# Optimization experiments

Hardware: AMD Instinct MI355X
Metric: run time of the kernel (lower is better)

Reference implementation:

```python
import jax, jax.numpy as jnp
import numpy as np

N = 50000      # nodes
E = 800000     # edges (avg degree 16)
DIN = 128
DOUT = 128
L = 8          # num GCN2Conv layers
ALPHA = 0.1
THETA = 0.5


def setup_inputs() -> dict:
    key = jax.random.key(0)
    ks = jax.random.split(key, 5)
    x = jax.random.normal(ks[0], (N, DIN), jnp.float32)
    edge_index = jax.random.randint(ks[1], (2, E), 0, N, dtype=jnp.int64)
    # pre-normalized adjacency weights (normalize=False in GCN2Conv -> adj_t already normalized)
    edge_weight = jax.random.uniform(ks[2], (E,), jnp.float32) / 16.0
    W_lin = jax.random.normal(ks[3], (DIN, DOUT), jnp.float32) / np.sqrt(DIN).astype(np.float32)
    b_lin = jnp.zeros((DOUT,), jnp.float32)
    W_convs = jax.random.normal(ks[4], (L, DOUT, DOUT), jnp.float32) / np.sqrt(DOUT).astype(np.float32)
    return {"x": x, "edge_weight": edge_weight, "W_lin": W_lin, "b_lin": b_lin,
            "W_convs": W_convs, "edge_index": edge_index}


def reference(x, edge_weight, W_lin, b_lin, W_convs, edge_index):
    src, dst = edge_index[0], edge_index[1]
    # betas for GCN2Conv layer l (1-indexed): beta_l = log(theta/l + 1)
    betas = np.log(THETA / np.arange(1, L + 1) + 1.0).astype(np.float32)
    # x = lins(x).relu(); dropout p=0 is a no-op
    x0 = jax.nn.relu(x @ W_lin + b_lin)          # [N, DOUT]
    h = x0
    for l in range(L):
        # sparse propagate: agg = A @ h  (SpMM via gather + segment_sum)
        agg = jax.ops.segment_sum(h[src] * edge_weight[:, None], dst, num_segments=N)
        # initial-residual mixing
        m = (1.0 - ALPHA) * agg + ALPHA * x0
        # identity mapping (shared_weights): out = (1-beta)*m + beta*(m @ W)
        h = jax.nn.relu((1.0 - betas[l]) * m + betas[l] * (m @ W_convs[l]))
    return h
```

## Files before the change

### kernel.cpp

```cpp
#include <hip/hip_runtime.h>
#include <math.h>

#define N_NODES 50000
#define N_EDGES 800000
#define DIM 128
#define SCAN_BLOCKS 49

typedef __attribute__((ext_vector_type(8))) short short8;
typedef __attribute__((ext_vector_type(4))) float floatx4;

__device__ __forceinline__ unsigned short f32_to_bf16(float f) {
    unsigned int u = __float_as_uint(f);
    u += 0x7fffu + ((u >> 16) & 1u);
    return (unsigned short)(u >> 16);
}
__device__ __forceinline__ float bf16_to_f32(unsigned short h) {
    return __uint_as_float((unsigned int)h << 16);
}


__global__ __launch_bounds__(256) void hist_kernel(const int* __restrict__ dst,
                                                   int* __restrict__ deg) {
    int e = blockIdx.x * 256 + threadIdx.x;
    if (e < N_EDGES) atomicAdd(&deg[dst[e]], 1);
}

__global__ __launch_bounds__(1024) void scan1(const int* __restrict__ deg,
                                              int* __restrict__ rowp,
                                              int* __restrict__ part) {
    __shared__ int buf[1024];
    int i = blockIdx.x * 1024 + threadIdx.x;
    int v = (i < N_NODES) ? deg[i] : 0;
    buf[threadIdx.x] = v;
    __syncthreads();
    for (int off = 1; off < 1024; off <<= 1) {
        int t = (threadIdx.x >= (unsigned)off) ? buf[threadIdx.x - off] : 0;
        __syncthreads();
        buf[threadIdx.x] += t;
        __syncthreads();
    }
    if (i < N_NODES) rowp[i] = buf[threadIdx.x] - v;
    if (threadIdx.x == 1023) part[blockIdx.x] = buf[1023];
}

__global__ void scan2(int* __restrict__ part) {
    int v = (threadIdx.x < SCAN_BLOCKS) ? part[threadIdx.x] : 0;
    for (int off = 1; off < 64; off <<= 1) {
        int t = __shfl_up(v, off);
        if ((int)threadIdx.x >= off) v += t;
    }
    if (threadIdx.x < SCAN_BLOCKS) part[threadIdx.x] = v;
}

__global__ __launch_bounds__(1024) void scan3(int* __restrict__ rowp,
                                              int* __restrict__ cursor,
                                              const int* __restrict__ part) {
    int i = blockIdx.x * 1024 + threadIdx.x;
    int off = (blockIdx.x > 0) ? part[blockIdx.x - 1] : 0;
    if (i < N_NODES) {
        int r = rowp[i] + off;
        rowp[i] = r;
        cursor[i] = r;
    }
    if (i == N_NODES) rowp[N_NODES] = part[SCAN_BLOCKS - 1];
}

__global__ __launch_bounds__(256) void scatter_kernel(const int* __restrict__ src,
                                                      const int* __restrict__ dst,
                                                      const float* __restrict__ ew,
                                                      int* __restrict__ cursor,
                                                      int2* __restrict__ ep) {
    int e = blockIdx.x * 256 + threadIdx.x;
    if (e < N_EDGES) {
        int d = dst[e];
        int pos = atomicAdd(&cursor[d], 1);
        int2 p; p.x = src[e]; p.y = __float_as_int(ew[e]);
        ep[pos] = p;
    }
}


__global__ __launch_bounds__(256) void spmm7(const unsigned short* __restrict__ hB,
                                             const unsigned short* __restrict__ x0B,
                                             const int* __restrict__ rowp,
                                             const int2* __restrict__ ep,
                                             unsigned short* __restrict__ mB) {
    int node = blockIdx.x * 4 + (threadIdx.x >> 6);
    int lane = threadIdx.x & 63;
    int eg = lane >> 4;
    int fb = (lane & 15) * 8;
    int beg = rowp[node], end = rowp[node + 1];
    float acc[8] = {0.f, 0.f, 0.f, 0.f, 0.f, 0.f, 0.f, 0.f};
    if (beg < end) {
        int last = end - 1;
        for (int i = beg; i < end; i += 16) {
            int i0 = i + eg, i1 = i0 + 4, i2 = i0 + 8, i3 = i0 + 12;
            int2 e0 = ep[min(i0, last)];
            int2 e1 = ep[min(i1, last)];
            int2 e2 = ep[min(i2, last)];
            int2 e3 = ep[min(i3, last)];
            short8 r0 = *(const short8*)(const void*)(hB + (size_t)e0.x * DIM + fb);
            short8 r1 = *(const short8*)(const void*)(hB + (size_t)e1.x * DIM + fb);
            short8 r2 = *(const short8*)(const void*)(hB + (size_t)e2.x * DIM + fb);
            short8 r3 = *(const short8*)(const void*)(hB + (size_t)e3.x * DIM + fb);
            float w0 = (i0 < end) ? __int_as_float(e0.y) : 0.f;
            float w1 = (i1 < end) ? __int_as_float(e1.y) : 0.f;
            float w2 = (i2 < end) ? __int_as_float(e2.y) : 0.f;
            float w3 = (i3 < end) ? __int_as_float(e3.y) : 0.f;
#pragma unroll
            for (int j = 0; j < 8; j++) {
                acc[j] = fmaf(w0, bf16_to_f32((unsigned short)r0[j]), acc[j]);
                acc[j] = fmaf(w1, bf16_to_f32((unsigned short)r1[j]), acc[j]);
                acc[j] = fmaf(w2, bf16_to_f32((unsigned short)r2[j]), acc[j]);
                acc[j] = fmaf(w3, bf16_to_f32((unsigned short)r3[j]), acc[j]);
            }
        }
    }
#pragma unroll
    for (int j = 0; j < 8; j++) {
        acc[j] += __shfl_down(acc[j], 32);
        acc[j] += __shfl_down(acc[j], 16);
    }
    if (lane < 16) {
        size_t off = (size_t)node * DIM + fb;
        short8 xv = *(const short8*)(const void*)(x0B + off);
        short8 o;
#pragma unroll
        for (int j = 0; j < 8; j++)
            o[j] = (short)f32_to_bf16(0.9f * acc[j]
                                      + 0.1f * bf16_to_f32((unsigned short)xv[j]));
        *(short8*)(void*)(mB + off) = o;
    }
}


template <bool AF32>
__global__ __launch_bounds__(256) void gemm128(const void* __restrict__ Av,
                                               const float* __restrict__ W,
                                               const float* __restrict__ bias,
                                               float* __restrict__ outF,
                                               unsigned short* __restrict__ outB,
                                               float cm, float cg) {
    __shared__ unsigned short WT[128][136];
    for (int idx = threadIdx.x; idx < 128 * 128; idx += 256) {
        int k = idx >> 7, n = idx & 127;
        float wv = cg * W[idx] + ((n == k) ? cm : 0.f);
        WT[n][k] = f32_to_bf16(wv);
    }
    __syncthreads();

    int wave = threadIdx.x >> 6;
    int lane = threadIdx.x & 63;
    int r0 = (blockIdx.x * 4 + wave) * 16;
    if (r0 >= N_NODES) return;

    int mrow = lane & 15;
    int quad = lane >> 4;

    floatx4 acc[8];
#pragma unroll
    for (int t = 0; t < 8; t++) acc[t] = {0.f, 0.f, 0.f, 0.f};

#pragma unroll
    for (int k0 = 0; k0 < 128; k0 += 32) {
        short8 a;
        if constexpr (AF32) {
            const float* arow = (const float*)Av + (size_t)(r0 + mrow) * DIM;
            floatx4 alo = *(const floatx4*)(const void*)(arow + k0 + quad * 8);
            floatx4 ahi = *(const floatx4*)(const void*)(arow + k0 + quad * 8 + 4);
#pragma unroll
            for (int j = 0; j < 4; j++) a[j] = (short)f32_to_bf16(alo[j]);
#pragma unroll
            for (int j = 0; j < 4; j++) a[4 + j] = (short)f32_to_bf16(ahi[j]);
        } else {
            const unsigned short* arow = (const unsigned short*)Av + (size_t)(r0 + mrow) * DIM;
            a = *(const short8*)(const void*)(arow + k0 + quad * 8);
        }
#pragma unroll
        for (int t = 0; t < 8; t++) {
            short8 b = *(const short8*)(const void*)(&WT[t * 16 + mrow][k0 + quad * 8]);
            acc[t] = __builtin_amdgcn_mfma_f32_16x16x32_bf16(a, b, acc[t], 0, 0, 0);
        }
    }

#pragma unroll
    for (int t = 0; t < 8; t++) {
        int col = t * 16 + mrow;
        float bv = bias ? bias[col] : 0.f;
#pragma unroll
        for (int i = 0; i < 4; i++) {
            int row = r0 + quad * 4 + i;
            size_t off = (size_t)row * DIM + col;
            float v = fmaxf(acc[t][i] + bv, 0.f);
            if (outF) outF[off] = v;
            if (outB) outB[off] = f32_to_bf16(v);
        }
    }
}


extern "C" void kernel_launch(void* const* d_in, const int* in_sizes, int n_in,
                              void* d_out, int out_size, void* d_ws, size_t ws_size,
                              hipStream_t stream) {
    const float* x    = (const float*)d_in[0];
    const float* ew   = (const float*)d_in[1];
    const float* Wlin = (const float*)d_in[2];
    const float* blin = (const float*)d_in[3];
    const float* Wcv  = (const float*)d_in[4];
    const int* eidx = (const int*)d_in[5];
    const int* esrc = eidx;
    const int* edst = eidx + N_EDGES;
    float* out = (float*)d_out;

    char* ws = (char*)d_ws;
    unsigned short* x0B = (unsigned short*)(ws);
    unsigned short* mB  = (unsigned short*)(ws + 12800000);
    unsigned short* hB  = (unsigned short*)(ws + 25600000);
    int* rowp           = (int*)(ws + 38400000);
    int* cursor         = (int*)(ws + 38600064);
    int2* epack         = (int2*)(ws + 38800128);
    int* part           = (int*)(ws + 45200128);

    (void)hipMemsetAsync(cursor, 0, (N_NODES + 1) * sizeof(int), stream);
    hist_kernel<<<(N_EDGES + 255) / 256, 256, 0, stream>>>(edst, cursor);
    scan1<<<SCAN_BLOCKS, 1024, 0, stream>>>(cursor, rowp, part);
    scan2<<<1, 64, 0, stream>>>(part);
    scan3<<<SCAN_BLOCKS, 1024, 0, stream>>>(rowp, cursor, part);
    scatter_kernel<<<(N_EDGES + 255) / 256, 256, 0, stream>>>(esrc, edst, ew, cursor, epack);

    const int grid = (N_NODES + 63) / 64;

    gemm128<true><<<grid, 256, 0, stream>>>(x, Wlin, blin, nullptr, x0B, 0.f, 1.f);

    const unsigned short* hin = x0B;
    for (int l = 0; l < 8; l++) {
        spmm7<<<N_NODES / 4, 256, 0, stream>>>(hin, x0B, rowp, epack, mB);
        float beta = logf(0.5f / (float)(l + 1) + 1.f);
        gemm128<false><<<grid, 256, 0, stream>>>(mB, Wcv + (size_t)l * DIM * DIM, nullptr,
                                                 (l == 7) ? out : nullptr,
                                                 (l < 7) ? hB : nullptr,
                                                 1.f - beta, beta);
        hin = hB;
    }
}
```

Before: 550.3 us.

## Fuse SpMM aggregation with per-layer GEMM and precompute bf16 layer weights

```diff
diff --git a/kernel.cpp b/kernel.cpp
--- a/kernel.cpp
+++ b/kernel.cpp
@@ -75,77 +75,126 @@
         int d = dst[e];
         int pos = atomicAdd(&cursor[d], 1);
         int2 p; p.x = src[e]; p.y = __float_as_int(ew[e]);
-        ep[pos] = p;
-    }
-}
-
-
-__global__ __launch_bounds__(256) void spmm7(const unsigned short* __restrict__ hB,
-                                             const unsigned short* __restrict__ x0B,
-                                             const int* __restrict__ rowp,
-                                             const int2* __restrict__ ep,
-                                             unsigned short* __restrict__ mB) {
-    int node = blockIdx.x * 4 + (threadIdx.x >> 6);
+        long long pv;
+        __builtin_memcpy(&pv, &p, 8);
+        __builtin_nontemporal_store(pv, (long long*)(ep + pos));
+    }
+}
+
+
+__global__ __launch_bounds__(256) void prep_wt(const float* __restrict__ Wcv,
+                                               unsigned short* __restrict__ WTall) {
+    int l = blockIdx.x;
+    float beta = logf(0.5f / (float)(l + 1) + 1.f);
+    float cm = 1.f - beta, cg = beta;
+    const float* W = Wcv + (size_t)l * DIM * DIM;
+    unsigned short* WT = WTall + (size_t)l * DIM * DIM;
+    for (int idx = threadIdx.x; idx < DIM * DIM; idx += 256) {
+        int k = idx >> 7, n = idx & 127;
+        WT[n * DIM + k] = f32_to_bf16(cg * W[idx] + ((n == k) ? cm : 0.f));
+    }
+}
+
+
+__global__ __launch_bounds__(256) void layer_fused(const unsigned short* __restrict__ hB,
+                                                   const unsigned short* __restrict__ x0B,
+                                                   const int* __restrict__ rowp,
+                                                   const int2* __restrict__ ep,
+                                                   const unsigned short* __restrict__ WT,
+                                                   float* __restrict__ outF,
+                                                   unsigned short* __restrict__ outB) {
+    __shared__ unsigned short M[16][136];
+    int wave = threadIdx.x >> 6;
     int lane = threadIdx.x & 63;
     int eg = lane >> 4;
     int fb = (lane & 15) * 8;
-    int beg = rowp[node], end = rowp[node + 1];
-    float acc[8] = {0.f, 0.f, 0.f, 0.f, 0.f, 0.f, 0.f, 0.f};
-    if (beg < end) {
-        int last = end - 1;
-        for (int i = beg; i < end; i += 16) {
-            int i0 = i + eg, i1 = i0 + 4, i2 = i0 + 8, i3 = i0 + 12;
-            int2 e0 = ep[min(i0, last)];
-            int2 e1 = ep[min(i1, last)];
-            int2 e2 = ep[min(i2, last)];
-            int2 e3 = ep[min(i3, last)];
-            short8 r0 = *(const short8*)(const void*)(hB + (size_t)e0.x * DIM + fb);
-            short8 r1 = *(const short8*)(const void*)(hB + (size_t)e1.x * DIM + fb);
-            short8 r2 = *(const short8*)(const void*)(hB + (size_t)e2.x * DIM + fb);
-            short8 r3 = *(const short8*)(const void*)(hB + (size_t)e3.x * DIM + fb);
-            float w0 = (i0 < end) ? __int_as_float(e0.y) : 0.f;
-            float w1 = (i1 < end) ? __int_as_float(e1.y) : 0.f;
-            float w2 = (i2 < end) ? __int_as_float(e2.y) : 0.f;
-            float w3 = (i3 < end) ? __int_as_float(e3.y) : 0.f;
-#pragma unroll
-            for (int j = 0; j < 8; j++) {
-                acc[j] = fmaf(w0, bf16_to_f32((unsigned short)r0[j]), acc[j]);
-                acc[j] = fmaf(w1, bf16_to_f32((unsigned short)r1[j]), acc[j]);
-                acc[j] = fmaf(w2, bf16_to_f32((unsigned short)r2[j]), acc[j]);
-                acc[j] = fmaf(w3, bf16_to_f32((unsigned short)r3[j]), acc[j]);
+    int nodeBase = blockIdx.x * 16;
+
+    for (int t = 0; t < 4; t++) {
+        int nl = wave * 4 + t;
+        int node = nodeBase + nl;
+        int beg = rowp[node], end = rowp[node + 1];
+        float acc[8] = {0.f, 0.f, 0.f, 0.f, 0.f, 0.f, 0.f, 0.f};
+        if (beg < end) {
+            int last = end - 1;
+            for (int i = beg; i < end; i += 16) {
+                int i0 = i + eg, i1 = i0 + 4, i2 = i0 + 8, i3 = i0 + 12;
+                int2 e0 = ep[min(i0, last)];
+                int2 e1 = ep[min(i1, last)];
+                int2 e2 = ep[min(i2, last)];
+                int2 e3 = ep[min(i3, last)];
+                short8 r0 = *(const short8*)(const void*)(hB + (size_t)e0.x * DIM + fb);
+                short8 r1 = *(const short8*)(const void*)(hB + (size_t)e1.x * DIM + fb);
+                short8 r2 = *(const short8*)(const void*)(hB + (size_t)e2.x * DIM + fb);
+                short8 r3 = *(const short8*)(const void*)(hB + (size_t)e3.x * DIM + fb);
+                float w0 = (i0 < end) ? __int_as_float(e0.y) : 0.f;
+                float w1 = (i1 < end) ? __int_as_float(e1.y) : 0.f;
+                float w2 = (i2 < end) ? __int_as_float(e2.y) : 0.f;
+                float w3 = (i3 < end) ? __int_as_float(e3.y) : 0.f;
+#pragma unroll
+                for (int j = 0; j < 8; j++) {
+                    acc[j] = fmaf(w0, bf16_to_f32((unsigned short)r0[j]), acc[j]);
+                    acc[j] = fmaf(w1, bf16_to_f32((unsigned short)r1[j]), acc[j]);
+                    acc[j] = fmaf(w2, bf16_to_f32((unsigned short)r2[j]), acc[j]);
+                    acc[j] = fmaf(w3, bf16_to_f32((unsigned short)r3[j]), acc[j]);
+                }
             }
         }
-    }
-#pragma unroll
-    for (int j = 0; j < 8; j++) {
-        acc[j] += __shfl_down(acc[j], 32);
-        acc[j] += __shfl_down(acc[j], 16);
-    }
-    if (lane < 16) {
-        size_t off = (size_t)node * DIM + fb;
-        short8 xv = *(const short8*)(const void*)(x0B + off);
-        short8 o;
-#pragma unroll
-        for (int j = 0; j < 8; j++)
-            o[j] = (short)f32_to_bf16(0.9f * acc[j]
-                                      + 0.1f * bf16_to_f32((unsigned short)xv[j]));
-        *(short8*)(void*)(mB + off) = o;
-    }
-}
-
-
-template <bool AF32>
-__global__ __launch_bounds__(256) void gemm128(const void* __restrict__ Av,
+#pragma unroll
+        for (int j = 0; j < 8; j++) {
+            acc[j] += __shfl_down(acc[j], 32);
+            acc[j] += __shfl_down(acc[j], 16);
+        }
+        if (lane < 16) {
+            short8 xv = *(const short8*)(const void*)(x0B + (size_t)(nodeBase + nl) * DIM + fb);
+            short8 o;
+#pragma unroll
+            for (int j = 0; j < 8; j++)
+                o[j] = (short)f32_to_bf16(0.9f * acc[j]
+                                          + 0.1f * bf16_to_f32((unsigned short)xv[j]));
+            *(short8*)(void*)(&M[nl][fb]) = o;
+        }
+    }
+    __syncthreads();
+
+    int mrow = lane & 15;
+    int quad = lane >> 4;
+    floatx4 acc2[2];
+    acc2[0] = {0.f, 0.f, 0.f, 0.f};
+    acc2[1] = {0.f, 0.f, 0.f, 0.f};
+#pragma unroll
+    for (int k0 = 0; k0 < 128; k0 += 32) {
+        short8 a = *(const short8*)(const void*)(&M[mrow][k0 + quad * 8]);
+#pragma unroll
+        for (int t = 0; t < 2; t++) {
+            int col = wave * 32 + t * 16 + mrow;
+            short8 b = *(const short8*)(const void*)(WT + (size_t)col * DIM + k0 + quad * 8);
+            acc2[t] = __builtin_amdgcn_mfma_f32_16x16x32_bf16(a, b, acc2[t], 0, 0, 0);
+        }
+    }
+#pragma unroll
+    for (int t = 0; t < 2; t++) {
+        int col = wave * 32 + t * 16 + mrow;
+#pragma unroll
+        for (int i = 0; i < 4; i++) {
+            int row = nodeBase + quad * 4 + i;
+            size_t off = (size_t)row * DIM + col;
+            float v = fmaxf(acc2[t][i], 0.f);
+            if (outF) outF[off] = v;
+            if (outB) outB[off] = f32_to_bf16(v);
+        }
+    }
+}
+
+
+__global__ __launch_bounds__(256) void gemm128(const float* __restrict__ A,
                                                const float* __restrict__ W,
                                                const float* __restrict__ bias,
-                                               float* __restrict__ outF,
-                                               unsigned short* __restrict__ outB,
-                                               float cm, float cg) {
-    __shared__ unsigned short WT[128][136];
+                                               unsigned short* __restrict__ outB) {
+    __shared__ unsigned short WTs[128][136];
     for (int idx = threadIdx.x; idx < 128 * 128; idx += 256) {
         int k = idx >> 7, n = idx & 127;
-        float wv = cg * W[idx] + ((n == k) ? cm : 0.f);
-        WT[n][k] = f32_to_bf16(wv);
+        WTs[n][k] = f32_to_bf16(W[idx]);
     }
     __syncthreads();
 
@@ -161,24 +210,19 @@
 #pragma unroll
     for (int t = 0; t < 8; t++) acc[t] = {0.f, 0.f, 0.f, 0.f};
 
+    const float* arow = A + (size_t)(r0 + mrow) * DIM;
 #pragma unroll
     for (int k0 = 0; k0 < 128; k0 += 32) {
+        floatx4 alo = *(const floatx4*)(const void*)(arow + k0 + quad * 8);
+        floatx4 ahi = *(const floatx4*)(const void*)(arow + k0 + quad * 8 + 4);
         short8 a;
-        if constexpr (AF32) {
-            const float* arow = (const float*)Av + (size_t)(r0 + mrow) * DIM;
-            floatx4 alo = *(const floatx4*)(const void*)(arow + k0 + quad * 8);
-            floatx4 ahi = *(const floatx4*)(const void*)(arow + k0 + quad * 8 + 4);
-#pragma unroll
-            for (int j = 0; j < 4; j++) a[j] = (short)f32_to_bf16(alo[j]);
-#pragma unroll
-            for (int j = 0; j < 4; j++) a[4 + j] = (short)f32_to_bf16(ahi[j]);
-        } else {
-            const unsigned short* arow = (const unsigned short*)Av + (size_t)(r0 + mrow) * DIM;
-            a = *(const short8*)(const void*)(arow + k0 + quad * 8);
-        }
+#pragma unroll
+        for (int j = 0; j < 4; j++) a[j] = (short)f32_to_bf16(alo[j]);
+#pragma unroll
+        for (int j = 0; j < 4; j++) a[4 + j] = (short)f32_to_bf16(ahi[j]);
 #pragma unroll
         for (int t = 0; t < 8; t++) {
-            short8 b = *(const short8*)(const void*)(&WT[t * 16 + mrow][k0 + quad * 8]);
+            short8 b = *(const short8*)(const void*)(&WTs[t * 16 + mrow][k0 + quad * 8]);
             acc[t] = __builtin_amdgcn_mfma_f32_16x16x32_bf16(a, b, acc[t], 0, 0, 0);
         }
     }
@@ -186,14 +230,12 @@
 #pragma unroll
     for (int t = 0; t < 8; t++) {
         int col = t * 16 + mrow;
-        float bv = bias ? bias[col] : 0.f;
+        float bv = bias[col];
 #pragma unroll
         for (int i = 0; i < 4; i++) {
             int row = r0 + quad * 4 + i;
-            size_t off = (size_t)row * DIM + col;
             float v = fmaxf(acc[t][i] + bv, 0.f);
-            if (outF) outF[off] = v;
-            if (outB) outB[off] = f32_to_bf16(v);
+            outB[(size_t)row * DIM + col] = f32_to_bf16(v);
         }
     }
 }
@@ -213,13 +255,14 @@
     float* out = (float*)d_out;
 
     char* ws = (char*)d_ws;
-    unsigned short* x0B = (unsigned short*)(ws);
-    unsigned short* mB  = (unsigned short*)(ws + 12800000);
-    unsigned short* hB  = (unsigned short*)(ws + 25600000);
-    int* rowp           = (int*)(ws + 38400000);
-    int* cursor         = (int*)(ws + 38600064);
-    int2* epack         = (int2*)(ws + 38800128);
-    int* part           = (int*)(ws + 45200128);
+    unsigned short* x0B  = (unsigned short*)(ws);
+    unsigned short* h0   = (unsigned short*)(ws + 12800000);
+    unsigned short* h1   = (unsigned short*)(ws + 25600000);
+    int* rowp            = (int*)(ws + 38400000);
+    int* cursor          = (int*)(ws + 38600064);
+    int2* epack          = (int2*)(ws + 38800128);
+    int* part            = (int*)(ws + 45200128);
+    unsigned short* WTall= (unsigned short*)(ws + 45200512);
 
     (void)hipMemsetAsync(cursor, 0, (N_NODES + 1) * sizeof(int), stream);
     hist_kernel<<<(N_EDGES + 255) / 256, 256, 0, stream>>>(edst, cursor);
@@ -227,19 +270,17 @@
     scan2<<<1, 64, 0, stream>>>(part);
     scan3<<<SCAN_BLOCKS, 1024, 0, stream>>>(rowp, cursor, part);
     scatter_kernel<<<(N_EDGES + 255) / 256, 256, 0, stream>>>(esrc, edst, ew, cursor, epack);
-
-    const int grid = (N_NODES + 63) / 64;
-
-    gemm128<true><<<grid, 256, 0, stream>>>(x, Wlin, blin, nullptr, x0B, 0.f, 1.f);
+    prep_wt<<<8, 256, 0, stream>>>(Wcv, WTall);
+
+    gemm128<<<(N_NODES + 63) / 64, 256, 0, stream>>>(x, Wlin, blin, x0B);
 
     const unsigned short* hin = x0B;
     for (int l = 0; l < 8; l++) {
-        spmm7<<<N_NODES / 4, 256, 0, stream>>>(hin, x0B, rowp, epack, mB);
-        float beta = logf(0.5f / (float)(l + 1) + 1.f);
-        gemm128<false><<<grid, 256, 0, stream>>>(mB, Wcv + (size_t)l * DIM * DIM, nullptr,
-                                                 (l == 7) ? out : nullptr,
-                                                 (l < 7) ? hB : nullptr,
-                                                 1.f - beta, beta);
-        hin = hB;
-    }
-}
+        unsigned short* hout = (l & 1) ? h1 : h0;
+        layer_fused<<<N_NODES / 16, 256, 0, stream>>>(hin, x0B, rowp, epack,
+                                                      WTall + (size_t)l * DIM * DIM,
+                                                      (l == 7) ? out : nullptr,
+                                                      (l < 7) ? hout : nullptr);
+        hin = hout;
+    }
+}
```

Measured after the change: 577.6 us. 1.05x slower.

## Precompute bf16 transposed weights once and fuse histogram with input GEMM

Applied to the files above, without the earlier changes.

```diff
diff --git a/kernel.cpp b/kernel.cpp
--- a/kernel.cpp
+++ b/kernel.cpp
@@ -5,6 +5,8 @@
 #define N_EDGES 800000
 #define DIM 128
 #define SCAN_BLOCKS 49
+#define HIST_BLOCKS 3125
+#define GEMM_BLOCKS 782
 
 typedef __attribute__((ext_vector_type(8))) short short8;
 typedef __attribute__((ext_vector_type(4))) float floatx4;
@@ -19,10 +21,97 @@
 }
 
 
-__global__ __launch_bounds__(256) void hist_kernel(const int* __restrict__ dst,
-                                                   int* __restrict__ deg) {
-    int e = blockIdx.x * 256 + threadIdx.x;
-    if (e < N_EDGES) atomicAdd(&deg[dst[e]], 1);
+__global__ __launch_bounds__(256) void prep_wt(const float* __restrict__ Wcv,
+                                               const float* __restrict__ Wlin,
+                                               unsigned short* __restrict__ WTall) {
+    int l = blockIdx.x;
+    const float* W;
+    float cm, cg;
+    if (l < 8) {
+        float beta = logf(0.5f / (float)(l + 1) + 1.f);
+        cm = 1.f - beta; cg = beta;
+        W = Wcv + (size_t)l * DIM * DIM;
+    } else {
+        cm = 0.f; cg = 1.f;
+        W = Wlin;
+    }
+    unsigned short* WT = WTall + (size_t)l * DIM * DIM;
+    for (int idx = threadIdx.x; idx < DIM * DIM; idx += 256) {
+        int k = idx >> 7, n = idx & 127;
+        WT[n * DIM + k] = f32_to_bf16(cg * W[idx] + ((n == k) ? cm : 0.f));
+    }
+}
+
+
+template <bool AF32>
+__device__ __forceinline__ void gemm_body(int bid, const void* __restrict__ Av,
+                                          const unsigned short* __restrict__ WT,
+                                          const float* __restrict__ bias,
+                                          float* __restrict__ outF,
+                                          unsigned short* __restrict__ outB) {
+    int wave = threadIdx.x >> 6;
+    int lane = threadIdx.x & 63;
+    int r0 = (bid * 4 + wave) * 16;
+    if (r0 >= N_NODES) return;
+
+    int mrow = lane & 15;
+    int quad = lane >> 4;
+
+    floatx4 acc[8];
+#pragma unroll
+    for (int t = 0; t < 8; t++) acc[t] = {0.f, 0.f, 0.f, 0.f};
+
+#pragma unroll
+    for (int k0 = 0; k0 < 128; k0 += 32) {
+        short8 a;
+        if constexpr (AF32) {
+            const float* arow = (const float*)Av + (size_t)(r0 + mrow) * DIM;
+            floatx4 alo = *(const floatx4*)(const void*)(arow + k0 + quad * 8);
+            floatx4 ahi = *(const floatx4*)(const void*)(arow + k0 + quad * 8 + 4);
+#pragma unroll
+            for (int j = 0; j < 4; j++) a[j] = (short)f32_to_bf16(alo[j]);
+#pragma unroll
+            for (int j = 0; j < 4; j++) a[4 + j] = (short)f32_to_bf16(ahi[j]);
+        } else {
+            const unsigned short* arow = (const unsigned short*)Av + (size_t)(r0 + mrow) * DIM;
+            a = *(const short8*)(const void*)(arow + k0 + quad * 8);
+        }
+#pragma unroll
+        for (int t = 0; t < 8; t++) {
+            short8 b = *(const short8*)(const void*)(WT + (size_t)(t * 16 + mrow) * DIM
+                                                     + k0 + quad * 8);
+            acc[t] = __builtin_amdgcn_mfma_f32_16x16x32_bf16(a, b, acc[t], 0, 0, 0);
+        }
+    }
+
+#pragma unroll
+    for (int t = 0; t < 8; t++) {
+        int col = t * 16 + mrow;
+        float bv = bias ? bias[col] : 0.f;
+#pragma unroll
+        for (int i = 0; i < 4; i++) {
+            int row = r0 + quad * 4 + i;
+            size_t off = (size_t)row * DIM + col;
+            float v = fmaxf(acc[t][i] + bv, 0.f);
+            if (outF) outF[off] = v;
+            if (outB) outB[off] = f32_to_bf16(v);
+        }
+    }
+}
+
+
+__global__ __launch_bounds__(256) void hist_gemm0(const int* __restrict__ dst,
+                                                  int* __restrict__ deg,
+                                                  const float* __restrict__ x,
+                                                  const unsigned short* __restrict__ WTlin,
+                                                  const float* __restrict__ bias,
+                                                  unsigned short* __restrict__ x0B) {
+    if (blockIdx.x < HIST_BLOCKS) {
+        int e = blockIdx.x * 256 + threadIdx.x;
+        if (e < N_EDGES) atomicAdd(&deg[dst[e]], 1);
+    } else {
+        gemm_body<true>(blockIdx.x - HIST_BLOCKS, x, WTlin, bias, nullptr, x0B);
+    }
 }
 
 __global__ __launch_bounds__(1024) void scan1(const int* __restrict__ deg,
@@ -134,68 +223,11 @@
 }
 
 
-template <bool AF32>
-__global__ __launch_bounds__(256) void gemm128(const void* __restrict__ Av,
-                                               const float* __restrict__ W,
-                                               const float* __restrict__ bias,
-                                               float* __restrict__ outF,
-                                               unsigned short* __restrict__ outB,
-                                               float cm, float cg) {
-    __shared__ unsigned short WT[128][136];
-    for (int idx = threadIdx.x; idx < 128 * 128; idx += 256) {
-        int k = idx >> 7, n = idx & 127;
-        float wv = cg * W[idx] + ((n == k) ? cm : 0.f);
-        WT[n][k] = f32_to_bf16(wv);
-    }
-    __syncthreads();
-
-    int wave = threadIdx.x >> 6;
-    int lane = threadIdx.x & 63;
-    int r0 = (blockIdx.x * 4 + wave) * 16;
-    if (r0 >= N_NODES) return;
-
-    int mrow = lane & 15;
-    int quad = lane >> 4;
-
-    floatx4 acc[8];
-#pragma unroll
-    for (int t = 0; t < 8; t++) acc[t] = {0.f, 0.f, 0.f, 0.f};
-
-#pragma unroll
-    for (int k0 = 0; k0 < 128; k0 += 32) {
-        short8 a;
-        if constexpr (AF32) {
-            const float* arow = (const float*)Av + (size_t)(r0 + mrow) * DIM;
-            floatx4 alo = *(const floatx4*)(const void*)(arow + k0 + quad * 8);
-            floatx4 ahi = *(const floatx4*)(const void*)(arow + k0 + quad * 8 + 4);
-#pragma unroll
-            for (int j = 0; j < 4; j++) a[j] = (short)f32_to_bf16(alo[j]);
-#pragma unroll
-            for (int j = 0; j < 4; j++) a[4 + j] = (short)f32_to_bf16(ahi[j]);
-        } else {
-            const unsigned short* arow = (const unsigned short*)Av + (size_t)(r0 + mrow) * DIM;
-            a = *(const short8*)(const void*)(arow + k0 + quad * 8);
-        }
-#pragma unroll
-        for (int t = 0; t < 8; t++) {
-            short8 b = *(const short8*)(const void*)(&WT[t * 16 + mrow][k0 + quad * 8]);
-            acc[t] = __builtin_amdgcn_mfma_f32_16x16x32_bf16(a, b, acc[t], 0, 0, 0);
-        }
-    }
-
-#pragma unroll
-    for (int t = 0; t < 8; t++) {
-        int col = t * 16 + mrow;
-        float bv = bias ? bias[col] : 0.f;
-#pragma unroll
-        for (int i = 0; i < 4; i++) {
-            int row = r0 + quad * 4 + i;
-            size_t off = (size_t)row * DIM + col;
-            float v = fmaxf(acc[t][i] + bv, 0.f);
-            if (outF) outF[off] = v;
-            if (outB) outB[off] = f32_to_bf16(v);
-        }
-    }
+__global__ __launch_bounds__(256) void gemm_layer(const unsigned short* __restrict__ A,
+                                                  const unsigned short* __restrict__ WT,
+                                                  float* __restrict__ outF,
+                                                  unsigned short* __restrict__ outB) {
+    gemm_body<false>(blockIdx.x, A, WT, nullptr, outF, outB);
 }
 
 
@@ -213,33 +245,31 @@
     float* out = (float*)d_out;
 
     char* ws = (char*)d_ws;
-    unsigned short* x0B = (unsigned short*)(ws);
-    unsigned short* mB  = (unsigned short*)(ws + 12800000);
-    unsigned short* hB  = (unsigned short*)(ws + 25600000);
-    int* rowp           = (int*)(ws + 38400000);
-    int* cursor         = (int*)(ws + 38600064);
-    int2* epack         = (int2*)(ws + 38800128);
-    int* part           = (int*)(ws + 45200128);
+    unsigned short* x0B  = (unsigned short*)(ws);
+    unsigned short* mB   = (unsigned short*)(ws + 12800000);
+    unsigned short* hB   = (unsigned short*)(ws + 25600000);
+    int* rowp            = (int*)(ws + 38400000);
+    int* cursor          = (int*)(ws + 38600064);
+    int2* epack          = (int2*)(ws + 38800128);
+    int* part            = (int*)(ws + 45200128);
+    unsigned short* WTall= (unsigned short*)(ws + 45200640);
+
+    prep_wt<<<9, 256, 0, stream>>>(Wcv, Wlin, WTall);
 
     (void)hipMemsetAsync(cursor, 0, (N_NODES + 1) * sizeof(int), stream);
-    hist_kernel<<<(N_EDGES + 255) / 256, 256, 0, stream>>>(edst, cursor);
+    hist_gemm0<<<HIST_BLOCKS + GEMM_BLOCKS, 256, 0, stream>>>(
+        edst, cursor, x, WTall + (size_t)8 * DIM * DIM, blin, x0B);
     scan1<<<SCAN_BLOCKS, 1024, 0, stream>>>(cursor, rowp, part);
     scan2<<<1, 64, 0, stream>>>(part);
     scan3<<<SCAN_BLOCKS, 1024, 0, stream>>>(rowp, cursor, part);
     scatter_kernel<<<(N_EDGES + 255) / 256, 256, 0, stream>>>(esrc, edst, ew, cursor, epack);
 
-    const int grid = (N_NODES + 63) / 64;
-
-    gemm128<true><<<grid, 256, 0, stream>>>(x, Wlin, blin, nullptr, x0B, 0.f, 1.f);
-
     const unsigned short* hin = x0B;
     for (int l = 0; l < 8; l++) {
         spmm7<<<N_NODES / 4, 256, 0, stream>>>(hin, x0B, rowp, epack, mB);
-        float beta = logf(0.5f / (float)(l + 1) + 1.f);
-        gemm128<false><<<grid, 256, 0, stream>>>(mB, Wcv + (size_t)l * DIM * DIM, nullptr,
-                                                 (l == 7) ? out : nullptr,
-                                                 (l < 7) ? hB : nullptr,
-                                                 1.f - beta, beta);
+        gemm_layer<<<GEMM_BLOCKS, 256, 0, stream>>>(mB, WTall + (size_t)l * DIM * DIM,
+                                                    (l == 7) ? out : nullptr,
+                                                    (l < 7) ? hB : nullptr);
         hin = hB;
     }
 }
```

Result: slower. 638.4 us (+16.0%).
